# Kernel tuning notes

Hardware: AMD Instinct MI355X
Metric: run time of the kernel (lower is better)

Reference implementation:

```python
import jax, jax.numpy as jnp
import numpy as np

N, E = 50000, 800000
D_IN, D_H, D_OUT = 128, 128, 128


def setup_inputs() -> dict:
    key = jax.random.key(0)
    ks = jax.random.split(key, 8)
    x = jax.random.normal(ks[0], (N, D_IN), dtype=jnp.float32)
    edge_index = jax.random.randint(ks[1], (2, E), 0, N, dtype=jnp.int64)
    s_in = 1.0 / np.sqrt(D_IN)
    s_h = 1.0 / np.sqrt(D_H)
    W1 = jax.random.normal(ks[2], (D_IN, D_H), dtype=jnp.float32) * s_in
    b1 = jnp.zeros((D_H,), jnp.float32)
    Wg = jax.random.normal(ks[3], (D_H, D_H), dtype=jnp.float32) * s_h
    bg = jnp.zeros((D_H,), jnp.float32)
    W2 = jax.random.normal(ks[4], (D_H, D_OUT), dtype=jnp.float32) * s_h
    b2 = jnp.zeros((D_OUT,), jnp.float32)
    return {"x": x, "edge_index": edge_index, "W1": W1, "b1": b1,
            "Wg": Wg, "bg": bg, "W2": W2, "b2": b2}


def reference(x, edge_index, W1, b1, Wg, bg, W2, b2):
    # Linear -> ReLU
    h = jax.nn.relu(x @ W1 + b1)                      # [N, D_H]
    # GCNConv: transform, add self-loops, sym-normalize, scatter-aggregate
    h = h @ Wg                                        # [N, D_H]
    row, col = edge_index[0], edge_index[1]
    loop = jnp.arange(N, dtype=edge_index.dtype)
    row = jnp.concatenate([row, loop])                # [E+N] sources
    col = jnp.concatenate([col, loop])                # [E+N] targets
    deg = jax.ops.segment_sum(jnp.ones(E + N, h.dtype), col, num_segments=N)
    dinv = jnp.where(deg > 0, jax.lax.rsqrt(deg), 0.0)
    norm = dinv[row] * dinv[col]                      # [E+N]
    agg = jax.ops.segment_sum(h[row] * norm[:, None], col, num_segments=N)
    agg = agg + bg                                    # GCNConv bias
    # ReLU -> Linear
    return jax.nn.relu(agg) @ W2 + b2                 # [N, D_OUT]
```

## Files before the change

### kernel.cpp

```cpp
#include <hip/hip_runtime.h>

#define D 128

typedef short bf16x8 __attribute__((ext_vector_type(8)));
typedef float f32x4 __attribute__((ext_vector_type(4)));

static __device__ __forceinline__ unsigned int f2bf(float f) {
  unsigned int u = __float_as_uint(f);
  return (u + 0x7FFFu + ((u >> 16) & 1u)) >> 16;
}
static __device__ __forceinline__ unsigned int pack2bf(float lo, float hi) {
  return f2bf(lo) | (f2bf(hi) << 16);
}
static __device__ __forceinline__ float bf_lo(unsigned int v) {
  return __uint_as_float(v << 16);
}
static __device__ __forceinline__ float bf_hi(unsigned int v) {
  return __uint_as_float(v & 0xFFFF0000u);
}


__global__ __launch_bounds__(256) void k_zero(int* __restrict__ p, int n) {
  int i = blockIdx.x * 256 + threadIdx.x;
  if (i < n) p[i] = 0;
}

__global__ __launch_bounds__(256) void k_fill(const int* __restrict__ ei, int E,
                                              int* __restrict__ deg,
                                              unsigned short* __restrict__ csr16,
                                              int cap, int T) {
  int e0 = blockIdx.x * 256 + threadIdx.x;
  int e1 = e0 + T;
  bool v0 = e0 < E, v1 = e1 < E;
  int r0 = 0, c0 = 0, r1 = 0, c1 = 0;
  if (v0) { r0 = __builtin_nontemporal_load(ei + e0); c0 = __builtin_nontemporal_load(ei + E + e0); }
  if (v1) { r1 = __builtin_nontemporal_load(ei + e1); c1 = __builtin_nontemporal_load(ei + E + e1); }
  int p0 = 0, p1 = 0;
  if (v0) p0 = atomicAdd(&deg[c0], 1);
  if (v1) p1 = atomicAdd(&deg[c1], 1);
  if (v0 && p0 < cap) csr16[(size_t)c0 * cap + p0] = (unsigned short)r0;
  if (v1 && p1 < cap) csr16[(size_t)c1 * cap + p1] = (unsigned short)r1;
}

__global__ __launch_bounds__(256) void k_dinv(const int* __restrict__ deg, int N,
                                              float* __restrict__ dinv) {
  int n = blockIdx.x * 256 + threadIdx.x;
  if (n < N) dinv[n] = rsqrtf((float)(deg[n] + 1));
}


__global__ __launch_bounds__(256) void k_wcvt(const float* __restrict__ W1,
                                              const float* __restrict__ Wg,
                                              const float* __restrict__ W2,
                                              unsigned short* __restrict__ WT) {
  const float* W = (blockIdx.x == 0) ? W1 : (blockIdx.x == 1) ? Wg : W2;
  unsigned short* T = WT + blockIdx.x * 16384;
  for (int idx = threadIdx.x; idx < 16384; idx += 256) {
    int k = idx >> 7, j = idx & 127;
    T[j * 128 + k] = (unsigned short)f2bf(W[idx]);
  }
}


__global__ __launch_bounds__(256) void k_mlp(const float* __restrict__ x,
                                             const unsigned short* __restrict__ W1T,
                                             const float* __restrict__ b1,
                                             const unsigned short* __restrict__ WgT,
                                             const float* __restrict__ dinv,
                                             unsigned short* __restrict__ h2, int N) {
  __shared__ unsigned short xs[64][136];
  __shared__ unsigned short wB[128][136];
  const int t = threadIdx.x;
  const int wave = t >> 6, lane = t & 63;
  const int rowBase = blockIdx.x * 64;
  const int ar = lane & 15, kg = lane >> 4;

#pragma unroll
  for (int i = 0; i < 8; ++i) {
    int idx = t + i * 256;
    int r = idx >> 5, c4 = (idx & 31) << 2;
    float4 v = make_float4(0.f, 0.f, 0.f, 0.f);
    int gr = rowBase + r;
    if (gr < N) v = *(const float4*)(x + (size_t)gr * D + c4);
    *(unsigned int*)&xs[r][c4]     = pack2bf(v.x, v.y);
    *(unsigned int*)&xs[r][c4 + 2] = pack2bf(v.z, v.w);
  }
#pragma unroll
  for (int i = 0; i < 8; ++i) {
    int idx = t + i * 256;
    int r = idx >> 4, c8 = (idx & 15) << 3;
    *(uint4*)&wB[r][c8] = *(const uint4*)(W1T + r * 128 + c8);
  }
  __syncthreads();

  float bias1[8];
#pragma unroll
  for (int cf = 0; cf < 8; ++cf) bias1[cf] = b1[cf * 16 + ar];
  float dnv[4];
#pragma unroll
  for (int reg = 0; reg < 4; ++reg) {
    int gr = rowBase + wave * 16 + 4 * kg + reg;
    dnv[reg] = (gr < N) ? dinv[gr] : 0.f;
  }

  f32x4 acc[8];
#pragma unroll
  for (int cf = 0; cf < 8; ++cf) acc[cf] = (f32x4){0.f, 0.f, 0.f, 0.f};
#pragma unroll
  for (int ks = 0; ks < 4; ++ks) {
    bf16x8 a = *(const bf16x8*)&xs[wave * 16 + ar][ks * 32 + kg * 8];
#pragma unroll
    for (int cf = 0; cf < 8; ++cf) {
      bf16x8 b = *(const bf16x8*)&wB[cf * 16 + ar][ks * 32 + kg * 8];
      acc[cf] = __builtin_amdgcn_mfma_f32_16x16x32_bf16(a, b, acc[cf], 0, 0, 0);
    }
  }

#pragma unroll
  for (int cf = 0; cf < 8; ++cf)
#pragma unroll
    for (int reg = 0; reg < 4; ++reg) {
      float v = fmaxf(acc[cf][reg] + bias1[cf], 0.f);
      xs[wave * 16 + 4 * kg + reg][cf * 16 + ar] = (unsigned short)f2bf(v);
    }
  __syncthreads();

#pragma unroll
  for (int i = 0; i < 8; ++i) {
    int idx = t + i * 256;
    int r = idx >> 4, c8 = (idx & 15) << 3;
    *(uint4*)&wB[r][c8] = *(const uint4*)(WgT + r * 128 + c8);
  }
  __syncthreads();

#pragma unroll
  for (int cf = 0; cf < 8; ++cf) acc[cf] = (f32x4){0.f, 0.f, 0.f, 0.f};
#pragma unroll
  for (int ks = 0; ks < 4; ++ks) {
    bf16x8 a = *(const bf16x8*)&xs[wave * 16 + ar][ks * 32 + kg * 8];
#pragma unroll
    for (int cf = 0; cf < 8; ++cf) {
      bf16x8 b = *(const bf16x8*)&wB[cf * 16 + ar][ks * 32 + kg * 8];
      acc[cf] = __builtin_amdgcn_mfma_f32_16x16x32_bf16(a, b, acc[cf], 0, 0, 0);
    }
  }

#pragma unroll
  for (int cf = 0; cf < 8; ++cf)
#pragma unroll
    for (int reg = 0; reg < 4; ++reg) {
      int gr = rowBase + wave * 16 + 4 * kg + reg;
      if (gr < N)
        h2[(size_t)gr * D + cf * 16 + ar] = (unsigned short)f2bf(acc[cf][reg] * dnv[reg]);
    }
}


__global__ __launch_bounds__(256) void k_agg(const unsigned short* __restrict__ h2,
                                             const int* __restrict__ deg,
                                             const unsigned short* __restrict__ csr16,
                                             const float* __restrict__ dinv,
                                             const float* __restrict__ bg,
                                             float* __restrict__ agg, int N, int cap) {
  int wave = threadIdx.x >> 6;
  int lane = threadIdx.x & 63;
  int n = blockIdx.x * 4 + wave;
  if (n >= N) return;
  const unsigned int* h2v = (const unsigned int*)h2;
  unsigned int vself = h2v[(size_t)n * 64 + lane];
  float dn = dinv[n];
  float2 bgv = ((const float2*)bg)[lane];
  float ax = 0.f, ay = 0.f;
  int cnt = min(deg[n], cap);
  size_t base = (size_t)n * cap;
  int i = 0;
  for (; i + 16 <= cnt; i += 16) {
    uint4 pa = *(const uint4*)(csr16 + base + i);
    uint4 pb = *(const uint4*)(csr16 + base + i + 8);
    int s[16] = {(int)(pa.x & 0xFFFFu), (int)(pa.x >> 16),
                 (int)(pa.y & 0xFFFFu), (int)(pa.y >> 16),
                 (int)(pa.z & 0xFFFFu), (int)(pa.z >> 16),
                 (int)(pa.w & 0xFFFFu), (int)(pa.w >> 16),
                 (int)(pb.x & 0xFFFFu), (int)(pb.x >> 16),
                 (int)(pb.y & 0xFFFFu), (int)(pb.y >> 16),
                 (int)(pb.z & 0xFFFFu), (int)(pb.z >> 16),
                 (int)(pb.w & 0xFFFFu), (int)(pb.w >> 16)};
    unsigned int v[16];
#pragma unroll
    for (int u = 0; u < 16; ++u) v[u] = h2v[(size_t)s[u] * 64 + lane];
#pragma unroll
    for (int u = 0; u < 16; ++u) { ax += bf_lo(v[u]); ay += bf_hi(v[u]); }
  }
  for (; i + 8 <= cnt; i += 8) {
    uint4 pk = *(const uint4*)(csr16 + base + i);
    int s[8] = {(int)(pk.x & 0xFFFFu), (int)(pk.x >> 16),
                (int)(pk.y & 0xFFFFu), (int)(pk.y >> 16),
                (int)(pk.z & 0xFFFFu), (int)(pk.z >> 16),
                (int)(pk.w & 0xFFFFu), (int)(pk.w >> 16)};
    unsigned int v[8];
#pragma unroll
    for (int u = 0; u < 8; ++u) v[u] = h2v[(size_t)s[u] * 64 + lane];
#pragma unroll
    for (int u = 0; u < 8; ++u) { ax += bf_lo(v[u]); ay += bf_hi(v[u]); }
  }
  for (; i < cnt; ++i) {
    int s = csr16[base + i];
    unsigned int v = h2v[(size_t)s * 64 + lane];
    ax += bf_lo(v); ay += bf_hi(v);
  }
  ax += bf_lo(vself); ay += bf_hi(vself);
  float2 o;
  o.x = fmaxf(fmaf(ax, dn, bgv.x), 0.f);
  o.y = fmaxf(fmaf(ay, dn, bgv.y), 0.f);
  ((float2*)agg)[(size_t)n * 64 + lane] = o;
}


__global__ __launch_bounds__(256) void k_out(const float* __restrict__ a,
                                             const unsigned short* __restrict__ W2T,
                                             const float* __restrict__ b2,
                                             float* __restrict__ out, int N) {
  __shared__ unsigned short xs[64][136];
  __shared__ unsigned short wB[128][136];
  const int t = threadIdx.x;
  const int wave = t >> 6, lane = t & 63;
  const int rowBase = blockIdx.x * 64;
  const int ar = lane & 15, kg = lane >> 4;

#pragma unroll
  for (int i = 0; i < 8; ++i) {
    int idx = t + i * 256;
    int r = idx >> 5, c4 = (idx & 31) << 2;
    float4 v = make_float4(0.f, 0.f, 0.f, 0.f);
    int gr = rowBase + r;
    if (gr < N) v = *(const float4*)(a + (size_t)gr * D + c4);
    *(unsigned int*)&xs[r][c4]     = pack2bf(v.x, v.y);
    *(unsigned int*)&xs[r][c4 + 2] = pack2bf(v.z, v.w);
  }
#pragma unroll
  for (int i = 0; i < 8; ++i) {
    int idx = t + i * 256;
    int r = idx >> 4, c8 = (idx & 15) << 3;
    *(uint4*)&wB[r][c8] = *(const uint4*)(W2T + r * 128 + c8);
  }
  __syncthreads();

  float bias2[8];
#pragma unroll
  for (int cf = 0; cf < 8; ++cf) bias2[cf] = b2[cf * 16 + ar];

  f32x4 acc[8];
#pragma unroll
  for (int cf = 0; cf < 8; ++cf) acc[cf] = (f32x4){0.f, 0.f, 0.f, 0.f};
#pragma unroll
  for (int ks = 0; ks < 4; ++ks) {
    bf16x8 a8 = *(const bf16x8*)&xs[wave * 16 + ar][ks * 32 + kg * 8];
#pragma unroll
    for (int cf = 0; cf < 8; ++cf) {
      bf16x8 b8 = *(const bf16x8*)&wB[cf * 16 + ar][ks * 32 + kg * 8];
      acc[cf] = __builtin_amdgcn_mfma_f32_16x16x32_bf16(a8, b8, acc[cf], 0, 0, 0);
    }
  }

#pragma unroll
  for (int cf = 0; cf < 8; ++cf)
#pragma unroll
    for (int reg = 0; reg < 4; ++reg) {
      int gr = rowBase + wave * 16 + 4 * kg + reg;
      if (gr < N)
        out[(size_t)gr * D + cf * 16 + ar] = acc[cf][reg] + bias2[cf];
    }
}


extern "C" void kernel_launch(void* const* d_in, const int* in_sizes, int n_in,
                              void* d_out, int out_size, void* d_ws, size_t ws_size,
                              hipStream_t stream) {
  const float* x  = (const float*)d_in[0];
  const int*   ei = (const int*)d_in[1];
  const float* W1 = (const float*)d_in[2];
  const float* b1 = (const float*)d_in[3];
  const float* Wg = (const float*)d_in[4];
  const float* bg = (const float*)d_in[5];
  const float* W2 = (const float*)d_in[6];
  const float* b2 = (const float*)d_in[7];
  const int N = in_sizes[0] / D;
  const int E = in_sizes[1] / 2;
  float* out = (float*)d_out;

  unsigned short* h2 = (unsigned short*)d_ws;
  unsigned short* WT = h2 + (size_t)N * D;
  float* dinv = (float*)(WT + 3 * 16384);
  int*   deg  = (int*)(dinv + N);
  unsigned short* csr16 = (unsigned short*)(deg + N);

  size_t fixed = (size_t)N * D * 2 + 3 * 16384 * 2 + (size_t)N * 8;
  int cap;
  if (ws_size >= fixed + (size_t)N * 64 * 2)      cap = 64;
  else if (ws_size >= fixed + (size_t)N * 48 * 2) cap = 48;
  else return;

  const int FB = 2048;
  const int FT = FB * 256;

  k_zero<<<(N + 255) / 256, 256, 0, stream>>>(deg, N);
  k_fill<<<FB, 256, 0, stream>>>(ei, E, deg, csr16, cap, FT);
  k_dinv<<<(N + 255) / 256, 256, 0, stream>>>(deg, N, dinv);
  k_wcvt<<<3, 256, 0, stream>>>(W1, Wg, W2, WT);
  k_mlp <<<(N + 63) / 64, 256, 0, stream>>>(x, WT, b1, WT + 16384, dinv, h2, N);
  k_agg <<<(N + 3) / 4, 256, 0, stream>>>(h2, deg, csr16, dinv, bg, out, N, cap);
  k_out <<<(N + 63) / 64, 256, 0, stream>>>(out, WT + 2 * 16384, b2, out, N);
}
```

Measured before the change: 142.4 us.

## Merge prep kernels, inline dinv, and partition CSR fill by target residue

Merges the weight conversion and degree zeroing into one prep kernel and drops the separate dinv kernel, so consumers compute rsqrt(deg+1) inline. This removes two launches and one buffer. The fill kernel now splits edges into 2048-edge chunks handled by 8 blocks each, and each block only inserts edges whose target mod 8 matches its index. The aim is to localize atomics and CSR writes, at the cost of every block re-reading the target indices 8 times.

```diff
diff --git a/kernel.cpp b/kernel.cpp
--- a/kernel.cpp
+++ b/kernel.cpp
@@ -20,44 +20,49 @@
 }
 
 
-__global__ __launch_bounds__(256) void k_zero(int* __restrict__ p, int n) {
-  int i = blockIdx.x * 256 + threadIdx.x;
-  if (i < n) p[i] = 0;
-}
+__global__ __launch_bounds__(256) void k_prep(const float* __restrict__ W1,
+                                              const float* __restrict__ Wg,
+                                              const float* __restrict__ W2,
+                                              unsigned short* __restrict__ WT,
+                                              int* __restrict__ deg, int N) {
+  if (blockIdx.x < 3) {
+    const float* W = (blockIdx.x == 0) ? W1 : (blockIdx.x == 1) ? Wg : W2;
+    unsigned short* T = WT + blockIdx.x * 16384;
+    for (int idx = threadIdx.x; idx < 16384; idx += 256) {
+      int k = idx >> 7, j = idx & 127;
+      T[j * 128 + k] = (unsigned short)f2bf(W[idx]);
+    }
+  } else {
+    int i = (blockIdx.x - 3) * 256 + threadIdx.x;
+    if (i < N) deg[i] = 0;
+  }
+}
+
+
+#define FILL_CHUNK 2048
 
 __global__ __launch_bounds__(256) void k_fill(const int* __restrict__ ei, int E,
                                               int* __restrict__ deg,
                                               unsigned short* __restrict__ csr16,
-                                              int cap, int T) {
-  int e0 = blockIdx.x * 256 + threadIdx.x;
-  int e1 = e0 + T;
-  bool v0 = e0 < E, v1 = e1 < E;
-  int r0 = 0, c0 = 0, r1 = 0, c1 = 0;
-  if (v0) { r0 = __builtin_nontemporal_load(ei + e0); c0 = __builtin_nontemporal_load(ei + E + e0); }
-  if (v1) { r1 = __builtin_nontemporal_load(ei + e1); c1 = __builtin_nontemporal_load(ei + E + e1); }
-  int p0 = 0, p1 = 0;
-  if (v0) p0 = atomicAdd(&deg[c0], 1);
-  if (v1) p1 = atomicAdd(&deg[c1], 1);
-  if (v0 && p0 < cap) csr16[(size_t)c0 * cap + p0] = (unsigned short)r0;
-  if (v1 && p1 < cap) csr16[(size_t)c1 * cap + p1] = (unsigned short)r1;
-}
-
-__global__ __launch_bounds__(256) void k_dinv(const int* __restrict__ deg, int N,
-                                              float* __restrict__ dinv) {
-  int n = blockIdx.x * 256 + threadIdx.x;
-  if (n < N) dinv[n] = rsqrtf((float)(deg[n] + 1));
-}
-
-
-__global__ __launch_bounds__(256) void k_wcvt(const float* __restrict__ W1,
-                                              const float* __restrict__ Wg,
-                                              const float* __restrict__ W2,
-                                              unsigned short* __restrict__ WT) {
-  const float* W = (blockIdx.x == 0) ? W1 : (blockIdx.x == 1) ? Wg : W2;
-  unsigned short* T = WT + blockIdx.x * 16384;
-  for (int idx = threadIdx.x; idx < 16384; idx += 256) {
-    int k = idx >> 7, j = idx & 127;
-    T[j * 128 + k] = (unsigned short)f2bf(W[idx]);
+                                              int cap) {
+  const int p = blockIdx.x & 7;
+  const int base = (blockIdx.x >> 3) * FILL_CHUNK;
+  const int t = threadIdx.x;
+  int c[8];
+#pragma unroll
+  for (int u = 0; u < 8; ++u) {
+    int e = base + u * 256 + t;
+    c[u] = (e < E) ? ei[E + e] : -1;
+  }
+#pragma unroll
+  for (int u = 0; u < 8; ++u) {
+    if (c[u] >= 0 && (c[u] & 7) == p) {
+      int e = base + u * 256 + t;
+      int r = ei[e];
+      int pos = atomicAdd(&deg[c[u]], 1);
+      if (pos < cap)
+        csr16[(size_t)c[u] * cap + pos] = (unsigned short)r;
+    }
   }
 }
 
@@ -66,7 +71,7 @@
                                              const unsigned short* __restrict__ W1T,
                                              const float* __restrict__ b1,
                                              const unsigned short* __restrict__ WgT,
-                                             const float* __restrict__ dinv,
+                                             const int* __restrict__ deg,
                                              unsigned short* __restrict__ h2, int N) {
   __shared__ unsigned short xs[64][136];
   __shared__ unsigned short wB[128][136];
@@ -100,7 +105,7 @@
 #pragma unroll
   for (int reg = 0; reg < 4; ++reg) {
     int gr = rowBase + wave * 16 + 4 * kg + reg;
-    dnv[reg] = (gr < N) ? dinv[gr] : 0.f;
+    dnv[reg] = (gr < N) ? rsqrtf((float)(deg[gr] + 1)) : 0.f;
   }
 
   f32x4 acc[8];
@@ -159,7 +164,6 @@
 __global__ __launch_bounds__(256) void k_agg(const unsigned short* __restrict__ h2,
                                              const int* __restrict__ deg,
                                              const unsigned short* __restrict__ csr16,
-                                             const float* __restrict__ dinv,
                                              const float* __restrict__ bg,
                                              float* __restrict__ agg, int N, int cap) {
   int wave = threadIdx.x >> 6;
@@ -168,10 +172,11 @@
   if (n >= N) return;
   const unsigned int* h2v = (const unsigned int*)h2;
   unsigned int vself = h2v[(size_t)n * 64 + lane];
-  float dn = dinv[n];
+  int dg = deg[n];
   float2 bgv = ((const float2*)bg)[lane];
+  float dn = rsqrtf((float)(dg + 1));
   float ax = 0.f, ay = 0.f;
-  int cnt = min(deg[n], cap);
+  int cnt = min(dg, cap);
   size_t base = (size_t)n * cap;
   int i = 0;
   for (; i + 16 <= cnt; i += 16) {
@@ -290,24 +295,21 @@
 
   unsigned short* h2 = (unsigned short*)d_ws;
   unsigned short* WT = h2 + (size_t)N * D;
-  float* dinv = (float*)(WT + 3 * 16384);
-  int*   deg  = (int*)(dinv + N);
+  int*   deg  = (int*)(WT + 3 * 16384);
   unsigned short* csr16 = (unsigned short*)(deg + N);
 
-  size_t fixed = (size_t)N * D * 2 + 3 * 16384 * 2 + (size_t)N * 8;
+  size_t fixed = (size_t)N * D * 2 + 3 * 16384 * 2 + (size_t)N * 4;
   int cap;
   if (ws_size >= fixed + (size_t)N * 64 * 2)      cap = 64;
   else if (ws_size >= fixed + (size_t)N * 48 * 2) cap = 48;
   else return;
 
-  const int FB = 2048;
-  const int FT = FB * 256;
-
-  k_zero<<<(N + 255) / 256, 256, 0, stream>>>(deg, N);
-  k_fill<<<FB, 256, 0, stream>>>(ei, E, deg, csr16, cap, FT);
-  k_dinv<<<(N + 255) / 256, 256, 0, stream>>>(deg, N, dinv);
-  k_wcvt<<<3, 256, 0, stream>>>(W1, Wg, W2, WT);
-  k_mlp <<<(N + 63) / 64, 256, 0, stream>>>(x, WT, b1, WT + 16384, dinv, h2, N);
-  k_agg <<<(N + 3) / 4, 256, 0, stream>>>(h2, deg, csr16, dinv, bg, out, N, cap);
+  const int nzb = (N + 255) / 256;
+  const int fillb = ((E + FILL_CHUNK - 1) / FILL_CHUNK) * 8;
+
+  k_prep<<<3 + nzb, 256, 0, stream>>>(W1, Wg, W2, WT, deg, N);
+  k_fill<<<fillb, 256, 0, stream>>>(ei, E, deg, csr16, cap);
+  k_mlp <<<(N + 63) / 64, 256, 0, stream>>>(x, WT, b1, WT + 16384, deg, h2, N);
+  k_agg <<<(N + 3) / 4, 256, 0, stream>>>(h2, deg, csr16, bg, out, N, cap);
   k_out <<<(N + 63) / 64, 256, 0, stream>>>(out, WT + 2 * 16384, b2, out, N);
 }
```

New measurement: 131.6 us. 1.08x faster.
